# Kernel optimization log

Measured on AMD Instinct MI355X. Metric: run time of the kernel, lower is better.

The kernel has to match this reference:

```python
import jax, jax.numpy as jnp
import numpy as np

DIM = 512
HEADS = 8
ALPHA = 0.5
HIDDEN = int(DIM * 2.0)
EPS = 1e-5


def _layernorm(x, g, b):
    mu = jnp.mean(x, axis=-1, keepdims=True)
    var = jnp.var(x, axis=-1, keepdims=True)
    return (x - mu) * jax.lax.rsqrt(var + EPS) * g + b


def setup_inputs() -> dict:
    key = jax.random.key(0)
    ks = jax.random.split(key, 8)
    B, N, C = 4, 1536, DIM
    s = lambda fan_in: 1.0 / np.sqrt(fan_in)
    return {
        "x": jax.random.normal(ks[0], (B, N, C), dtype=jnp.float32),
        "ln1_g": jnp.ones((C,), jnp.float32),
        "ln1_b": jnp.zeros((C,), jnp.float32),
        "qkv_w": jax.random.normal(ks[1], (C, 3 * C), jnp.float32) * s(C),
        "qkv_b": jnp.zeros((3 * C,), jnp.float32),
        "ln2_g": jnp.ones((C,), jnp.float32),
        "ln2_b": jnp.zeros((C,), jnp.float32),
        "fc1_w": jax.random.normal(ks[2], (C, HIDDEN), jnp.float32) * s(C),
        "fc1_b": jnp.zeros((HIDDEN,), jnp.float32),
        "fc2_w": jax.random.normal(ks[3], (HIDDEN, C), jnp.float32) * s(HIDDEN),
        "fc2_b": jnp.zeros((C,), jnp.float32),
    }


def reference(x, ln1_g, ln1_b, qkv_w, qkv_b, ln2_g, ln2_b, fc1_w, fc1_b, fc2_w, fc2_b):
    B, N, C = x.shape
    H = HEADS
    d = C // H
    S = N // 3

    h = _layernorm(x, ln1_g, ln1_b)
    qkv = (h @ qkv_w + qkv_b).reshape(B, N, 3, H, d)
    qkv = jnp.transpose(qkv, (2, 0, 3, 1, 4))  # [3,B,H,N,d]
    q, k, v = qkv[0], qkv[1], qkv[2]

    attn = jnp.einsum('bhnd,bhmd->bhnm', q, k) * (d ** -0.5)  # [B,H,N,N]
    # sequential cross-segment score mixing (matches in-place torch semantics)
    s0 = attn[:, :, 0:S]
    s1 = attn[:, :, S:2 * S] + ALPHA * s0
    s2 = attn[:, :, 2 * S:] + ALPHA * s1
    attn = jnp.concatenate([s0, s1, s2], axis=2)
    attn = jax.nn.softmax(attn, axis=-1)

    o = jnp.einsum('bhnm,bhmd->bhnd', attn, v)
    o = jnp.transpose(o, (0, 2, 1, 3)).reshape(B, N, C)
    x = x + o  # NOTE: self.proj is defined but unused in the original forward

    h2 = _layernorm(x, ln2_g, ln2_b)
    m = jax.nn.gelu(h2 @ fc1_w + fc1_b, approximate=False) @ fc2_w + fc2_b
    return x + m
```

## Files before the change

### kernel.cpp

```cpp
#include <hip/hip_runtime.h>
#include <hip/hip_bf16.h>
#include <math.h>

#define DIMC 512
#define NSEQ 1536
#define BATCH 4
#define NHEADS 8
#define HDIM 64
#define SSEG 512
#define HIDDEN_DIM 1024
#define ALPHA_C 0.5f
#define EPS_C 1e-5f
#define NROWS (BATCH*NSEQ)
#define SHIFT_C 6.0f

typedef __attribute__((ext_vector_type(8))) short bfrag8;
typedef __attribute__((ext_vector_type(8))) _Float16 hfrag8;
typedef __attribute__((ext_vector_type(4))) float ffrag;
typedef float4 f4;

__device__ __forceinline__ ushort f2bf(float v) {
    __hip_bfloat16 hb = __float2bfloat16(v);
    return *(ushort*)&hb;
}

__device__ __forceinline__ void gl2lds16(const ushort* g, ushort* l) {
    __builtin_amdgcn_global_load_lds(
        (const __attribute__((address_space(1))) unsigned*)g,
        (__attribute__((address_space(3))) unsigned*)l, 16, 0, 0);
}

__global__ __launch_bounds__(256)
void prep_kernel(const float* __restrict__ qkv_w, const float* __restrict__ fc1_w,
                 const float* __restrict__ fc2_w, ushort* __restrict__ qkv_wt,
                 ushort* __restrict__ fc1_wt, ushort* __restrict__ fc2_wt,
                 const float* __restrict__ x, const float* __restrict__ g,
                 const float* __restrict__ bvec, ushort* __restrict__ h_out)
{
    int bid = blockIdx.x;
    if (bid < 448) {
        __shared__ float tile[64][65];
        const float* W; ushort* Wt; int K, N, n0, k0;
        if (bid < 192)      { W = qkv_w; Wt = qkv_wt; K = 512;  N = 1536; int b = bid;       n0 = (b % 24) * 64; k0 = (b / 24) * 64; }
        else if (bid < 320) { W = fc1_w; Wt = fc1_wt; K = 512;  N = 1024; int b = bid - 192; n0 = (b % 16) * 64; k0 = (b / 16) * 64; }
        else                { W = fc2_w; Wt = fc2_wt; K = 1024; N = 512;  int b = bid - 320; n0 = (b % 8)  * 64; k0 = (b / 8)  * 64; }
        int tx = threadIdx.x & 63, ty = threadIdx.x >> 6;
        #pragma unroll
        for (int i = 0; i < 16; i++) {
            int r = i * 4 + ty;
            tile[r][tx] = W[(size_t)(k0 + r) * N + n0 + tx];
        }
        __syncthreads();
        #pragma unroll
        for (int i = 0; i < 16; i++) {
            int r = i * 4 + ty;
            Wt[(size_t)(n0 + r) * K + k0 + tx] = f2bf(tile[tx][r]);
        }
    } else {
        __shared__ float red[16];
        int row = bid - 448;
        int t = threadIdx.x;
        int lane = t & 63, w = t >> 6;
        const float* rp = x + (size_t)row * DIMC;
        float v0 = rp[t];
        float v1 = rp[t + 256];
        float s = v0 + v1;
        float s2 = v0 * v0 + v1 * v1;
        #pragma unroll
        for (int o = 32; o > 0; o >>= 1) {
            s  += __shfl_down(s,  o, 64);
            s2 += __shfl_down(s2, o, 64);
        }
        if (lane == 0) { red[w] = s; red[8 + w] = s2; }
        __syncthreads();
        if (t == 0) {
            float a = red[0] + red[1] + red[2] + red[3];
            float c = red[8] + red[9] + red[10] + red[11];
            red[0] = a; red[8] = c;
        }
        __syncthreads();
        float mean = red[0] * (1.0f / DIMC);
        float var  = red[8] * (1.0f / DIMC) - mean * mean;
        float rstd = rsqrtf(var + EPS_C);
        ushort* op = h_out + (size_t)row * DIMC;
        op[t]       = f2bf((v0 - mean) * rstd * g[t]       + bvec[t]);
        op[t + 256] = f2bf((v1 - mean) * rstd * g[t + 256] + bvec[t + 256]);
    }
}

__global__ __launch_bounds__(256)
void ln_kernel(const float* __restrict__ in, const float* __restrict__ g,
               const float* __restrict__ b, ushort* __restrict__ out)
{
    __shared__ float red[16];
    int row = blockIdx.x;
    int t = threadIdx.x;
    int lane = t & 63, w = t >> 6;
    const float* rp = in + (size_t)row * DIMC;
    float v0 = rp[t];
    float v1 = rp[t + 256];
    float s = v0 + v1;
    float s2 = v0 * v0 + v1 * v1;
    #pragma unroll
    for (int o = 32; o > 0; o >>= 1) {
        s  += __shfl_down(s,  o, 64);
        s2 += __shfl_down(s2, o, 64);
    }
    if (lane == 0) { red[w] = s; red[8 + w] = s2; }
    __syncthreads();
    if (t == 0) {
        float a = red[0] + red[1] + red[2] + red[3];
        float c = red[8] + red[9] + red[10] + red[11];
        red[0] = a; red[8] = c;
    }
    __syncthreads();
    float mean = red[0] * (1.0f / DIMC);
    float var  = red[8] * (1.0f / DIMC) - mean * mean;
    float rstd = rsqrtf(var + EPS_C);
    ushort* op = out + (size_t)row * DIMC;
    op[t]       = f2bf((v0 - mean) * rstd * g[t]       + b[t]);
    op[t + 256] = f2bf((v1 - mean) * rstd * g[t + 256] + b[t + 256]);
}

template <int EPI>
__device__ __forceinline__
void mgemm_body(const ushort* __restrict__ A, const ushort* __restrict__ Wt,
                const float* __restrict__ bias, const float* resid,
                void* out, int M, int K, int Nn, int bx, int by,
                ushort* As, ushort* Bs)
{
    int tid = threadIdx.x;
    int lane = tid & 63, w = tid >> 6;
    int cl = lane & 15, qg = lane >> 4;
    int wm = w >> 1, wn = w & 1;
    int rowBase = by * 64, colBase = bx * 64;
    int sr = lane >> 2;
    int sb = (lane & 3) * 8;

    const ushort* agb = A  + (size_t)(rowBase + w * 16 + sr) * K + sb;
    const ushort* bgb = Wt + (size_t)(colBase + w * 16 + sr) * K + sb;

    ffrag acc[2][2];
    #pragma unroll
    for (int mi = 0; mi < 2; mi++)
        #pragma unroll
        for (int ni = 0; ni < 2; ni++)
            #pragma unroll
            for (int r = 0; r < 4; r++) acc[mi][ni][r] = 0.f;

    int niter = K >> 6;

    #pragma unroll
    for (int hf = 0; hf < 2; hf++) {
        gl2lds16(agb + hf * 32, As + (0 * 2 + hf) * 2048 + (w * 16) * 32);
        gl2lds16(bgb + hf * 32, Bs + (0 * 2 + hf) * 2048 + (w * 16) * 32);
    }
    __syncthreads();

    for (int it = 0; it < niter; it++) {
        int cur = it & 1;
        if (it + 1 < niter) {
            int k0 = (it + 1) * 64;
            #pragma unroll
            for (int hf = 0; hf < 2; hf++) {
                gl2lds16(agb + k0 + hf * 32, As + ((cur ^ 1) * 2 + hf) * 2048 + (w * 16) * 32);
                gl2lds16(bgb + k0 + hf * 32, Bs + ((cur ^ 1) * 2 + hf) * 2048 + (w * 16) * 32);
            }
        }
        #pragma unroll
        for (int ks = 0; ks < 2; ks++) {
            bfrag8 af[2], bf[2];
            #pragma unroll
            for (int mi = 0; mi < 2; mi++)
                af[mi] = *(const bfrag8*)&As[(cur * 2 + ks) * 2048 + (wm * 32 + mi * 16 + cl) * 32 + qg * 8];
            #pragma unroll
            for (int ni = 0; ni < 2; ni++)
                bf[ni] = *(const bfrag8*)&Bs[(cur * 2 + ks) * 2048 + (wn * 32 + ni * 16 + cl) * 32 + qg * 8];
            #pragma unroll
            for (int mi = 0; mi < 2; mi++)
                #pragma unroll
                for (int ni = 0; ni < 2; ni++)
                    acc[mi][ni] = __builtin_amdgcn_mfma_f32_16x16x32_bf16(af[mi], bf[ni], acc[mi][ni], 0, 0, 0);
        }
        if (it + 1 < niter) __syncthreads();
    }

    #pragma unroll
    for (int mi = 0; mi < 2; mi++) {
        #pragma unroll
        for (int ni = 0; ni < 2; ni++) {
            #pragma unroll
            for (int r = 0; r < 4; r++) {
                int row = rowBase + wm * 32 + mi * 16 + qg * 4 + r;
                int col = colBase + wn * 32 + ni * 16 + cl;
                float v = acc[mi][ni][r] + (EPI == 3 ? bias[row] : bias[col]);
                if (EPI == 1) v = 0.5f * v * (1.0f + erff(v * 0.70710678118654752f));
                if (EPI == 2) {
                    v += resid[(size_t)row * Nn + col];
                    ((float*)out)[(size_t)row * Nn + col] = v;
                } else if (EPI == 3) {
                    _Float16 e = (_Float16)v;
                    int t = col & 31;
                    int pcol = (col & ~31) | (((t & 15) >> 2) * 8 + (t >> 4) * 4 + (t & 3));
                    ((ushort*)out)[(size_t)row * Nn + pcol] = *(ushort*)&e;
                } else {
                    ((ushort*)out)[(size_t)row * Nn + col] = f2bf(v);
                }
            }
        }
    }
}

template <int EPI>
__global__ __launch_bounds__(256)
void mgemm_kernel(const ushort* __restrict__ A, const ushort* __restrict__ Wt,
                  const float* __restrict__ bias, const float* resid,
                  void* out, int M, int K, int Nn)
{
    __shared__ ushort As[2 * 2 * 64 * 32];
    __shared__ ushort Bs[2 * 2 * 64 * 32];
    mgemm_body<EPI>(A, Wt, bias, resid, out, M, K, Nn, blockIdx.x, blockIdx.y, As, Bs);
}

__global__ __launch_bounds__(256)
void qkvt_kernel(const ushort* __restrict__ h_bf, const ushort* __restrict__ qkv_wt,
                 const float* __restrict__ qkv_b, ushort* __restrict__ qkb,
                 ushort* __restrict__ vtb)
{
    __shared__ ushort As[2 * 2 * 64 * 32];
    __shared__ ushort Bs[2 * 2 * 64 * 32];
    int bid = blockIdx.x;
    if (bid < 1536) {
        mgemm_body<0>(h_bf, qkv_wt, qkv_b, nullptr, (void*)qkb,
                      NROWS, DIMC, 2 * DIMC, bid & 15, bid >> 4, As, Bs);
    } else {
        int b2 = bid - 1536;
        mgemm_body<3>(qkv_wt + (size_t)2 * DIMC * DIMC, h_bf, qkv_b + 2 * DIMC, nullptr,
                      (void*)vtb, DIMC, DIMC, NROWS, b2 % 96, b2 / 96, As, Bs);
    }
}

__global__ __launch_bounds__(256)
void attn_kernel(const ushort* __restrict__ qk, const ushort* __restrict__ vt,
                 const float* __restrict__ x, float* __restrict__ xres)
{
    __shared__ float Op[48][68];
    __shared__ float Lp[4][4][16][3];

    int n = blockIdx.x + (blockIdx.y << 5);
    int idx = n >> 3;
    int bh  = (n & 7) * 4 + (idx & 3);
    int qi0 = (idx >> 2) * 16;
    int b = bh >> 3, h = bh & 7;
    int tid = threadIdx.x;
    int lane = tid & 63, w = tid >> 6;
    int cl = lane & 15, qg = lane >> 4;

    const ushort* base = qk + (size_t)b * NSEQ * 1024 + h * HDIM;
    const _Float16* vbase = (const _Float16*)vt + (size_t)(h * HDIM) * NROWS + b * NSEQ;
    const float scale = 0.125f;

    bfrag8 bq[3][2];
    #pragma unroll
    for (int seg = 0; seg < 3; seg++)
        #pragma unroll
        for (int f = 0; f < 2; f++)
            bq[seg][f] = *(const bfrag8*)(base + (size_t)(seg * SSEG + qi0 + cl) * 1024 + f * 32 + qg * 8);

    ffrag o[3][4];
    #pragma unroll
    for (int seg = 0; seg < 3; seg++)
        #pragma unroll
        for (int mg = 0; mg < 4; mg++)
            #pragma unroll
            for (int r = 0; r < 4; r++) o[seg][mg][r] = 0.f;
    float lp[3] = {0.f, 0.f, 0.f};

    int kb = w * 384;

    auto loadf = [&](int k0, hfrag8* av, bfrag8 (*af)[2]) {
        #pragma unroll
        for (int mg = 0; mg < 4; mg++)
            av[mg] = *(const hfrag8*)(vbase + (size_t)(mg * 16 + cl) * NROWS + k0 + qg * 8);
        #pragma unroll
        for (int s = 0; s < 2; s++)
            #pragma unroll
            for (int f = 0; f < 2; f++)
                af[s][f] = *(const bfrag8*)(base + (size_t)(k0 + s * 16 + cl) * 1024 + 512 + f * 32 + qg * 8);
    };

    auto comp = [&](const hfrag8* av, const bfrag8 (*af)[2]) {
        float p[2][3][4];
        #pragma unroll
        for (int s = 0; s < 2; s++) {
            #pragma unroll
            for (int seg = 0; seg < 3; seg++) {
                ffrag c;
                #pragma unroll
                for (int r = 0; r < 4; r++) c[r] = 0.f;
                c = __builtin_amdgcn_mfma_f32_16x16x32_bf16(af[s][0], bq[seg][0], c, 0, 0, 0);
                c = __builtin_amdgcn_mfma_f32_16x16x32_bf16(af[s][1], bq[seg][1], c, 0, 0, 0);
                #pragma unroll
                for (int r = 0; r < 4; r++) p[s][seg][r] = c[r];
            }
        }
        #pragma unroll
        for (int s = 0; s < 2; s++) {
            #pragma unroll
            for (int r = 0; r < 4; r++) {
                float s0 = p[s][0][r] * scale;
                float s1 = p[s][1][r] * scale + ALPHA_C * s0;
                float s2 = p[s][2][r] * scale + ALPHA_C * s1;
                float e0 = __expf(s0 - SHIFT_C);
                float e1 = __expf(s1 - SHIFT_C);
                float e2 = __expf(s2 - SHIFT_C);
                p[s][0][r] = e0; p[s][1][r] = e1; p[s][2][r] = e2;
                lp[0] += e0; lp[1] += e1; lp[2] += e2;
            }
        }
        hfrag8 bp[3];
        #pragma unroll
        for (int seg = 0; seg < 3; seg++)
            #pragma unroll
            for (int j = 0; j < 4; j++) {
                bp[seg][j]     = (_Float16)p[0][seg][j];
                bp[seg][4 + j] = (_Float16)p[1][seg][j];
            }
        #pragma unroll
        for (int mg = 0; mg < 4; mg++)
            #pragma unroll
            for (int seg = 0; seg < 3; seg++)
                o[seg][mg] = __builtin_amdgcn_mfma_f32_16x16x32_f16(av[mg], bp[seg], o[seg][mg], 0, 0, 0);
    };

    hfrag8 avA[4], avB[4];
    bfrag8 afA[2][2], afB[2][2];
    loadf(kb, avA, afA);
    #pragma unroll 1
    for (int it = 0; it < 12; it += 2) {
        loadf(kb + (it + 1) * 32, avB, afB);
        comp(avA, afA);
        if (it + 2 < 12) loadf(kb + (it + 2) * 32, avA, afA);
        comp(avB, afB);
    }

    #pragma unroll
    for (int seg = 0; seg < 3; seg++) Lp[w][qg][cl][seg] = lp[seg];

    #pragma unroll 1
    for (int wv = 0; wv < 4; wv++) {
        __syncthreads();
        if (w == wv) {
            #pragma unroll
            for (int seg = 0; seg < 3; seg++)
                #pragma unroll
                for (int mg = 0; mg < 4; mg++) {
                    float* dst = &Op[seg * 16 + cl][mg * 16 + qg * 4];
                    if (wv == 0) {
                        #pragma unroll
                        for (int r = 0; r < 4; r++) dst[r] = o[seg][mg][r];
                    } else {
                        #pragma unroll
                        for (int r = 0; r < 4; r++) dst[r] += o[seg][mg][r];
                    }
                }
        }
    }
    __syncthreads();

    if (tid < 192) {
        int row = tid >> 2;
        int seg = row >> 4, q16 = row & 15;
        int d0 = (tid & 3) * 16;
        float l = 0.f;
        #pragma unroll
        for (int wv = 0; wv < 4; wv++)
            #pragma unroll
            for (int g2 = 0; g2 < 4; g2++)
                l += Lp[wv][g2][q16][seg];
        float invl = 1.0f / l;
        size_t rowg = ((size_t)(b * NSEQ + seg * SSEG + qi0 + q16)) * DIMC + h * HDIM + d0;
        #pragma unroll
        for (int dd = 0; dd < 16; dd += 4) {
            f4 xv = *(const f4*)(x + rowg + dd);
            f4 ov;
            ov.x = Op[row][d0 + dd + 0] * invl + xv.x;
            ov.y = Op[row][d0 + dd + 1] * invl + xv.y;
            ov.z = Op[row][d0 + dd + 2] * invl + xv.z;
            ov.w = Op[row][d0 + dd + 3] * invl + xv.w;
            *(f4*)(xres + rowg + dd) = ov;
        }
    }
}

extern "C" void kernel_launch(void* const* d_in, const int* in_sizes, int n_in,
                              void* d_out, int out_size, void* d_ws, size_t ws_size,
                              hipStream_t stream)
{
    const float* x     = (const float*)d_in[0];
    const float* ln1_g = (const float*)d_in[1];
    const float* ln1_b = (const float*)d_in[2];
    const float* qkv_w = (const float*)d_in[3];
    const float* qkv_b = (const float*)d_in[4];
    const float* ln2_g = (const float*)d_in[5];
    const float* ln2_b = (const float*)d_in[6];
    const float* fc1_w = (const float*)d_in[7];
    const float* fc1_b = (const float*)d_in[8];
    const float* fc2_w = (const float*)d_in[9];
    const float* fc2_b = (const float*)d_in[10];
    float* out = (float*)d_out;

    char* p = (char*)d_ws;
    ushort* h_bf    = (ushort*)p;  p += (size_t)NROWS * DIMC * 2;
    ushort* qkb     = (ushort*)p;  p += (size_t)NROWS * 2 * DIMC * 2;
    ushort* vtb     = (ushort*)p;  p += (size_t)DIMC * NROWS * 2;
    ushort* mid     = (ushort*)p;  p += (size_t)NROWS * HIDDEN_DIM * 2;
    ushort* qkv_wt  = (ushort*)p;  p += (size_t)3 * DIMC * DIMC * 2;
    ushort* fc1_wt  = (ushort*)p;  p += (size_t)HIDDEN_DIM * DIMC * 2;
    ushort* fc2_wt  = (ushort*)p;
    float* xres = out;

    prep_kernel<<<448 + NROWS, 256, 0, stream>>>(qkv_w, fc1_w, fc2_w, qkv_wt, fc1_wt, fc2_wt,
                                                 x, ln1_g, ln1_b, h_bf);

    qkvt_kernel<<<2304, 256, 0, stream>>>(h_bf, qkv_wt, qkv_b, qkb, vtb);

    attn_kernel<<<dim3(SSEG / 16, BATCH * NHEADS), 256, 0, stream>>>(qkb, vtb, x, xres);

    ln_kernel<<<NROWS, 256, 0, stream>>>(xres, ln2_g, ln2_b, h_bf);

    mgemm_kernel<1><<<dim3(HIDDEN_DIM / 64, NROWS / 64), 256, 0, stream>>>(
        h_bf, fc1_wt, fc1_b, nullptr, (void*)mid, NROWS, DIMC, HIDDEN_DIM);

    mgemm_kernel<2><<<dim3(DIMC / 64, NROWS / 64), 256, 0, stream>>>(
        mid, fc2_wt, fc2_b, xres, (void*)out, NROWS, HIDDEN_DIM, DIMC);
}
```

Before: 216.7 us.

## Load GEMM fragments directly from global memory into registers, dropping LDS staging

Replaces the LDS double-buffered global_load_lds staging in the shared GEMM body with direct per-wave global loads of MFMA fragments into registers, using two register buffers to software-pipeline across 128-wide K chunks. This removes shared memory use and the block barriers. In exchange, each wave reloads operand tiles that were previously shared across waves, which doubles global/L2 traffic, and register pressure rises from the large fragment buffers. Row-strided 16-byte loads also coalesce less well.

Measured after the change: 316.2 us. 1.46x slower.

```diff
diff --git a/kernel.cpp b/kernel.cpp
--- a/kernel.cpp
+++ b/kernel.cpp
@@ -24,12 +24,6 @@
     return *(ushort*)&hb;
 }
 
-__device__ __forceinline__ void gl2lds16(const ushort* g, ushort* l) {
-    __builtin_amdgcn_global_load_lds(
-        (const __attribute__((address_space(1))) unsigned*)g,
-        (__attribute__((address_space(3))) unsigned*)l, 16, 0, 0);
-}
-
 __global__ __launch_bounds__(256)
 void prep_kernel(const float* __restrict__ qkv_w, const float* __restrict__ fc1_w,
                  const float* __restrict__ fc2_w, ushort* __restrict__ qkv_wt,
@@ -126,19 +120,22 @@
 __device__ __forceinline__
 void mgemm_body(const ushort* __restrict__ A, const ushort* __restrict__ Wt,
                 const float* __restrict__ bias, const float* resid,
-                void* out, int M, int K, int Nn, int bx, int by,
-                ushort* As, ushort* Bs)
+                void* out, int M, int K, int Nn, int bx, int by)
 {
     int tid = threadIdx.x;
     int lane = tid & 63, w = tid >> 6;
     int cl = lane & 15, qg = lane >> 4;
     int wm = w >> 1, wn = w & 1;
-    int rowBase = by * 64, colBase = bx * 64;
-    int sr = lane >> 2;
-    int sb = (lane & 3) * 8;
-
-    const ushort* agb = A  + (size_t)(rowBase + w * 16 + sr) * K + sb;
-    const ushort* bgb = Wt + (size_t)(colBase + w * 16 + sr) * K + sb;
+    int rowBase = by * 64 + wm * 32, colBase = bx * 64 + wn * 32;
+
+    const ushort* ap[2];
+    const ushort* bp[2];
+    #pragma unroll
+    for (int mi = 0; mi < 2; mi++)
+        ap[mi] = A  + (size_t)(rowBase + mi * 16 + cl) * K + qg * 8;
+    #pragma unroll
+    for (int ni = 0; ni < 2; ni++)
+        bp[ni] = Wt + (size_t)(colBase + ni * 16 + cl) * K + qg * 8;
 
     ffrag acc[2][2];
     #pragma unroll
@@ -148,41 +145,35 @@
             #pragma unroll
             for (int r = 0; r < 4; r++) acc[mi][ni][r] = 0.f;
 
-    int niter = K >> 6;
-
-    #pragma unroll
-    for (int hf = 0; hf < 2; hf++) {
-        gl2lds16(agb + hf * 32, As + (0 * 2 + hf) * 2048 + (w * 16) * 32);
-        gl2lds16(bgb + hf * 32, Bs + (0 * 2 + hf) * 2048 + (w * 16) * 32);
-    }
-    __syncthreads();
-
-    for (int it = 0; it < niter; it++) {
-        int cur = it & 1;
-        if (it + 1 < niter) {
-            int k0 = (it + 1) * 64;
-            #pragma unroll
-            for (int hf = 0; hf < 2; hf++) {
-                gl2lds16(agb + k0 + hf * 32, As + ((cur ^ 1) * 2 + hf) * 2048 + (w * 16) * 32);
-                gl2lds16(bgb + k0 + hf * 32, Bs + ((cur ^ 1) * 2 + hf) * 2048 + (w * 16) * 32);
+    auto loadf = [&](int k0, bfrag8 (*fa)[2], bfrag8 (*fb)[2]) {
+        #pragma unroll
+        for (int ks = 0; ks < 4; ks++)
+            #pragma unroll
+            for (int mi = 0; mi < 2; mi++) {
+                fa[ks][mi] = *(const bfrag8*)(ap[mi] + k0 + ks * 32);
+                fb[ks][mi] = *(const bfrag8*)(bp[mi] + k0 + ks * 32);
             }
-        }
-        #pragma unroll
-        for (int ks = 0; ks < 2; ks++) {
-            bfrag8 af[2], bf[2];
-            #pragma unroll
-            for (int mi = 0; mi < 2; mi++)
-                af[mi] = *(const bfrag8*)&As[(cur * 2 + ks) * 2048 + (wm * 32 + mi * 16 + cl) * 32 + qg * 8];
-            #pragma unroll
-            for (int ni = 0; ni < 2; ni++)
-                bf[ni] = *(const bfrag8*)&Bs[(cur * 2 + ks) * 2048 + (wn * 32 + ni * 16 + cl) * 32 + qg * 8];
+    };
+    auto comp = [&](const bfrag8 (*fa)[2], const bfrag8 (*fb)[2]) {
+        #pragma unroll
+        for (int ks = 0; ks < 4; ks++)
             #pragma unroll
             for (int mi = 0; mi < 2; mi++)
                 #pragma unroll
                 for (int ni = 0; ni < 2; ni++)
-                    acc[mi][ni] = __builtin_amdgcn_mfma_f32_16x16x32_bf16(af[mi], bf[ni], acc[mi][ni], 0, 0, 0);
-        }
-        if (it + 1 < niter) __syncthreads();
+                    acc[mi][ni] = __builtin_amdgcn_mfma_f32_16x16x32_bf16(
+                        fa[ks][mi], fb[ks][ni], acc[mi][ni], 0, 0, 0);
+    };
+
+    bfrag8 faA[4][2], fbA[4][2], faB[4][2], fbB[4][2];
+    int nmac = K >> 7;
+    loadf(0, faA, fbA);
+    #pragma unroll 1
+    for (int it = 0; it < nmac; it += 2) {
+        if (it + 1 < nmac) loadf((it + 1) * 128, faB, fbB);
+        comp(faA, fbA);
+        if (it + 2 < nmac) loadf((it + 2) * 128, faA, fbA);
+        if (it + 1 < nmac) comp(faB, fbB);
     }
 
     #pragma unroll
@@ -191,8 +182,8 @@
         for (int ni = 0; ni < 2; ni++) {
             #pragma unroll
             for (int r = 0; r < 4; r++) {
-                int row = rowBase + wm * 32 + mi * 16 + qg * 4 + r;
-                int col = colBase + wn * 32 + ni * 16 + cl;
+                int row = rowBase + mi * 16 + qg * 4 + r;
+                int col = colBase + ni * 16 + cl;
                 float v = acc[mi][ni][r] + (EPI == 3 ? bias[row] : bias[col]);
                 if (EPI == 1) v = 0.5f * v * (1.0f + erff(v * 0.70710678118654752f));
                 if (EPI == 2) {
@@ -217,9 +208,7 @@
                   const float* __restrict__ bias, const float* resid,
                   void* out, int M, int K, int Nn)
 {
-    __shared__ ushort As[2 * 2 * 64 * 32];
-    __shared__ ushort Bs[2 * 2 * 64 * 32];
-    mgemm_body<EPI>(A, Wt, bias, resid, out, M, K, Nn, blockIdx.x, blockIdx.y, As, Bs);
+    mgemm_body<EPI>(A, Wt, bias, resid, out, M, K, Nn, blockIdx.x, blockIdx.y);
 }
 
 __global__ __launch_bounds__(256)
@@ -227,16 +216,14 @@
                  const float* __restrict__ qkv_b, ushort* __restrict__ qkb,
                  ushort* __restrict__ vtb)
 {
-    __shared__ ushort As[2 * 2 * 64 * 32];
-    __shared__ ushort Bs[2 * 2 * 64 * 32];
     int bid = blockIdx.x;
     if (bid < 1536) {
         mgemm_body<0>(h_bf, qkv_wt, qkv_b, nullptr, (void*)qkb,
-                      NROWS, DIMC, 2 * DIMC, bid & 15, bid >> 4, As, Bs);
+                      NROWS, DIMC, 2 * DIMC, bid & 15, bid >> 4);
     } else {
         int b2 = bid - 1536;
         mgemm_body<3>(qkv_wt + (size_t)2 * DIMC * DIMC, h_bf, qkv_b + 2 * DIMC, nullptr,
-                      (void*)vtb, DIMC, DIMC, NROWS, b2 % 96, b2 / 96, As, Bs);
+                      (void*)vtb, DIMC, DIMC, NROWS, b2 % 96, b2 / 96);
     }
 }
 
```
